# Kernel optimization log

Measured on AMD Instinct MI355X. Metric: run time of the kernel, lower is better.

The kernel has to match this reference:

```python
import jax, jax.numpy as jnp
import numpy as np

B, S, D, H = 2, 2048, 1024, 16
HD = D // H  # head_size = 64

def setup_inputs() -> dict:
    key = jax.random.key(0)
    ks = jax.random.split(key, 8)
    sc = 0.02
    return {
        "q": jax.random.normal(ks[0], (B, S, D), jnp.float32),
        "k": jax.random.normal(ks[1], (B, S, D), jnp.float32),
        "v": jax.random.normal(ks[2], (B, S, D), jnp.float32),
        "padding_mask": jnp.zeros((B, 1, 1, S), jnp.float32),
        "Wq": jax.random.normal(ks[3], (D, D), jnp.float32) * sc,
        "bq": jnp.zeros((D,), jnp.float32),
        "Wk": jax.random.normal(ks[4], (D, D), jnp.float32) * sc,
        "bk": jnp.zeros((D,), jnp.float32),
        "Wv": jax.random.normal(ks[5], (D, D), jnp.float32) * sc,
        "bv": jnp.zeros((D,), jnp.float32),
        "Wo": jax.random.normal(ks[6], (D, D), jnp.float32) * sc,
        "bo": jnp.zeros((D,), jnp.float32),
    }

def reference(q, k, v, padding_mask, Wq, bq, Wk, bk, Wv, bv, Wo, bo):
    b = q.shape[0]
    qh = (q @ Wq + bq).reshape(b, -1, H, HD)
    kh = (k @ Wk + bk).reshape(b, -1, H, HD)
    vh = (v @ Wv + bv).reshape(b, -1, H, HD)
    # [B, H, Sq, Sk] scores, materialized as in the original
    qk = jnp.einsum('bjhd,bkhd->bhjk', qh, kh) / jnp.sqrt(jnp.float32(HD))
    qk = qk + padding_mask * -1e12
    attn = jax.nn.softmax(qk, axis=-1)
    qkv = jnp.einsum('bhjk,bkhd->bjhd', attn, vh).reshape(b, -1, D)
    return qkv @ Wo + bo
```

## Files before the change

kernel.cpp:

```cpp
#include <hip/hip_runtime.h>
#include <math.h>

typedef __bf16 bf16_t;
typedef __bf16 bf16x8 __attribute__((ext_vector_type(8)));
typedef __bf16 bf16x4v __attribute__((ext_vector_type(4)));
typedef float f32x4 __attribute__((ext_vector_type(4)));
typedef float f32x16 __attribute__((ext_vector_type(16)));

#define LOG2E 1.4426950408889634f
#define MBIAS_C (-1e12f * LOG2E)

#if __has_builtin(__builtin_amdgcn_exp2f)
#define EXP2F(x) __builtin_amdgcn_exp2f(x)
#else
#define EXP2F(x) exp2f(x)
#endif

typedef __attribute__((address_space(1))) const unsigned int g_u32;
typedef __attribute__((address_space(3))) unsigned int l_u32;
__device__ __forceinline__ void load_lds_16B(const void* g, void* l){
  __builtin_amdgcn_global_load_lds((g_u32*)g, (l_u32*)l, 16, 0, 0);
}

__device__ __forceinline__ f32x16 zero16(){
  f32x16 z;
  #pragma unroll
  for (int i = 0; i < 16; i++) z[i] = 0.f;
  return z;
}

typedef union { bf16x4v b4; uint2 u2; } pk8;
typedef union { uint2 h[2]; bf16x8 b8; } pk16;
typedef union { float4 f4[4]; f32x16 v; } cinit_t;

__global__ __launch_bounds__(256) void cast3_kernel(const float* __restrict__ q,
                                                    const float* __restrict__ k,
                                                    const float* __restrict__ v,
                                                    bf16_t* __restrict__ out){
  int z = blockIdx.y;
  const float* x = (z == 0) ? q : (z == 1) ? k : v;
  int i = blockIdx.x * 256 + threadIdx.x;
  float4 f = reinterpret_cast<const float4*>(x)[i];
  bf16x4v w;
  w[0] = (bf16_t)f.x; w[1] = (bf16_t)f.y; w[2] = (bf16_t)f.z; w[3] = (bf16_t)f.w;
  reinterpret_cast<bf16x4v*>(out + (size_t)z * 4194304)[i] = w;
}

__global__ __launch_bounds__(256) void mask_scale_kernel(const float* __restrict__ mask,
                                                         float* __restrict__ ms){
  int i = blockIdx.x * 256 + threadIdx.x;
  ms[i] = mask[i] * MBIAS_C;
}

__global__ __launch_bounds__(256) void wtrans4_kernel(const float* __restrict__ Wq,
                                                      const float* __restrict__ Wk,
                                                      const float* __restrict__ Wv,
                                                      const float* __restrict__ Wo,
                                                      bf16_t* __restrict__ Wcat,
                                                      bf16_t* __restrict__ Wot){
  __shared__ float T[32][33];
  int z = blockIdx.z;
  const float* W = (z == 0) ? Wq : (z == 1) ? Wk : (z == 2) ? Wv : Wo;
  bf16_t* dst = (z < 3) ? (Wcat + (size_t)z * 1024 * 1024) : Wot;
  int x = threadIdx.x, y = threadIdx.y;
  int k0 = blockIdx.y * 32, n0 = blockIdx.x * 32;
  #pragma unroll
  for (int i = 0; i < 4; i++) T[y + 8*i][x] = W[(size_t)(k0 + y + 8*i) * 1024 + n0 + x];
  __syncthreads();
  #pragma unroll
  for (int i = 0; i < 4; i++) dst[(size_t)(n0 + y + 8*i) * 1024 + k0 + x] = (bf16_t)T[x][y + 8*i];
}

__device__ __forceinline__ void qkv_epilogue(f32x4 (&acc)[4][4], int seg, int n0g, int m0,
                                             int wm, int wn, int l16, int lq,
                                             const float* bias, bf16_t* qp, bf16_t* kp,
                                             bf16_t* vh){
  bf16_t* Cp = (seg == 0) ? qp : (seg == 1) ? kp : vh;
  float scale = (seg == 0) ? 0.125f * LOG2E : 1.0f;
  #pragma unroll
  for (int ti = 0; ti < 4; ti++){
    #pragma unroll
    for (int tj = 0; tj < 4; tj++){
      int col = (n0g + wn + tj*16 + l16) & 1023;
      float bvv = bias[col];
      #pragma unroll
      for (int r = 0; r < 4; r++){
        int row = m0 + wm + ti*16 + lq*4 + r;
        Cp[(size_t)row * 1024 + col] = (bf16_t)((acc[ti][tj][r] + bvv) * scale);
      }
    }
  }
}

__global__ __launch_bounds__(256) void gemm_qkv_bf(const bf16_t* __restrict__ qkvin,
                                                   const bf16_t* __restrict__ Wcat,
                                                   const float* __restrict__ bq,
                                                   const float* __restrict__ bk,
                                                   const float* __restrict__ bv,
                                                   bf16_t* __restrict__ qp,
                                                   bf16_t* __restrict__ kp,
                                                   bf16_t* __restrict__ vh){
  const int K = 1024;
  __shared__ __align__(16) bf16_t As[128*32];
  __shared__ __align__(16) bf16_t Bs[128*32];
  int tid = threadIdx.x, wave = tid >> 6, lane = tid & 63;
  int l16 = lane & 15, lq = lane >> 4;
  int n0g = blockIdx.x * 128;
  int seg = n0g >> 10;
  const bf16_t* A   = qkvin + (size_t)seg * 4194304;
  const float* bias = (seg == 0) ? bq : (seg == 1) ? bk : bv;
  int m0 = blockIdx.y * 128;
  int wm = (wave >> 1) * 64, wn = (wave & 1) * 64;
  int cposR = lq ^ ((l16 >> 2) & 3);
  f32x4 acc[4][4] = {};
  for (int kt = 0; kt < K; kt += 32){
    __syncthreads();
    #pragma unroll
    for (int i = 0; i < 2; i++){
      int u = tid + 256*i;
      int r = u >> 2, cpos = u & 3, cg = cpos ^ ((r >> 2) & 3);
      int ldsoff = (wave*64 + 256*i) * 16;
      load_lds_16B(&A[(size_t)(m0 + r) * K + kt + cg*8], (char*)As + ldsoff);
      load_lds_16B(&Wcat[(size_t)(n0g + r) * K + kt + cg*8], (char*)Bs + ldsoff);
    }
    __syncthreads();
    bf16x8 af[4], bfr[4];
    #pragma unroll
    for (int t = 0; t < 4; t++) af[t]  = *reinterpret_cast<bf16x8*>(&As[(wm + t*16 + l16)*32 + cposR*8]);
    #pragma unroll
    for (int t = 0; t < 4; t++) bfr[t] = *reinterpret_cast<bf16x8*>(&Bs[(wn + t*16 + l16)*32 + cposR*8]);
    #pragma unroll
    for (int ti = 0; ti < 4; ti++)
      #pragma unroll
      for (int tj = 0; tj < 4; tj++)
        acc[ti][tj] = __builtin_amdgcn_mfma_f32_16x16x32_bf16(af[ti], bfr[tj], acc[ti][tj], 0, 0, 0);
  }
  qkv_epilogue(acc, seg, n0g, m0, wm, wn, l16, lq, bias, qp, kp, vh);
}

__global__ __launch_bounds__(256) void gemm_qkv_f32(const float* __restrict__ qi,
                                                    const float* __restrict__ ki,
                                                    const float* __restrict__ vi,
                                                    const bf16_t* __restrict__ Wcat,
                                                    const float* __restrict__ bq,
                                                    const float* __restrict__ bk,
                                                    const float* __restrict__ bv,
                                                    bf16_t* __restrict__ qp,
                                                    bf16_t* __restrict__ kp,
                                                    bf16_t* __restrict__ vh){
  const int K = 1024;
  __shared__ __align__(16) float  Asf[128*32];
  __shared__ __align__(16) bf16_t Bs[128*32];
  int tid = threadIdx.x, wave = tid >> 6, lane = tid & 63;
  int l16 = lane & 15, lq = lane >> 4;
  int n0g = blockIdx.x * 128;
  int seg = n0g >> 10;
  const float* A    = (seg == 0) ? qi : (seg == 1) ? ki : vi;
  const float* bias = (seg == 0) ? bq : (seg == 1) ? bk : bv;
  int m0 = blockIdx.y * 128;
  int wm = (wave >> 1) * 64, wn = (wave & 1) * 64;
  int cposR = lq ^ ((l16 >> 2) & 3);
  int ca0 = (2*lq)     ^ (l16 & 7);
  int ca1 = (2*lq + 1) ^ (l16 & 7);
  f32x4 acc[4][4] = {};
  for (int kt = 0; kt < K; kt += 32){
    __syncthreads();
    #pragma unroll
    for (int i = 0; i < 4; i++){
      int u = tid + 256*i;
      int r = u >> 3, cpos = u & 7, cg = cpos ^ (r & 7);
      load_lds_16B(&A[(size_t)(m0 + r) * K + kt + cg*4], (char*)Asf + (wave*64 + 256*i)*16);
    }
    #pragma unroll
    for (int i = 0; i < 2; i++){
      int u = tid + 256*i;
      int r = u >> 2, cpos = u & 3, cg = cpos ^ ((r >> 2) & 3);
      load_lds_16B(&Wcat[(size_t)(n0g + r) * K + kt + cg*8], (char*)Bs + (wave*64 + 256*i)*16);
    }
    __syncthreads();
    bf16x8 af[4], bfr[4];
    #pragma unroll
    for (int t = 0; t < 4; t++){
      int row = wm + t*16 + l16;
      f32x4 x0 = *reinterpret_cast<f32x4*>(&Asf[row*32 + ca0*4]);
      f32x4 x1 = *reinterpret_cast<f32x4*>(&Asf[row*32 + ca1*4]);
      bf16x8 a;
      a[0] = (bf16_t)x0[0]; a[1] = (bf16_t)x0[1]; a[2] = (bf16_t)x0[2]; a[3] = (bf16_t)x0[3];
      a[4] = (bf16_t)x1[0]; a[5] = (bf16_t)x1[1]; a[6] = (bf16_t)x1[2]; a[7] = (bf16_t)x1[3];
      af[t] = a;
    }
    #pragma unroll
    for (int t = 0; t < 4; t++) bfr[t] = *reinterpret_cast<bf16x8*>(&Bs[(wn + t*16 + l16)*32 + cposR*8]);
    #pragma unroll
    for (int ti = 0; ti < 4; ti++)
      #pragma unroll
      for (int tj = 0; tj < 4; tj++)
        acc[ti][tj] = __builtin_amdgcn_mfma_f32_16x16x32_bf16(af[ti], bfr[tj], acc[ti][tj], 0, 0, 0);
  }
  qkv_epilogue(acc, seg, n0g, m0, wm, wn, l16, lq, bias, qp, kp, vh);
}

__global__ __launch_bounds__(256) void gemm_out(const bf16_t* __restrict__ A,
                                                const bf16_t* __restrict__ Bt,
                                                const float* __restrict__ bias,
                                                float* __restrict__ C){
  const int K = 1024, N = 1024;
  __shared__ __align__(16) bf16_t As[128*64];
  __shared__ __align__(16) bf16_t Bs[64*64];
  int tid = threadIdx.x, wave = tid >> 6, lane = tid & 63;
  int l16 = lane & 15, lq = lane >> 4;
  int m0 = blockIdx.y * 128, n0 = blockIdx.x * 64;
  int wm = wave * 32;
  f32x4 acc[2][4] = {};
  for (int kt = 0; kt < K; kt += 64){
    __syncthreads();
    #pragma unroll
    for (int i = 0; i < 4; i++){
      int u = tid + 256*i;
      int r = u >> 3, cpos = u & 7, cg = cpos ^ (r & 7);
      load_lds_16B(&A[(size_t)(m0 + r) * K + kt + cg*8], (char*)As + (wave*64 + 256*i)*16);
    }
    #pragma unroll
    for (int i = 0; i < 2; i++){
      int u = tid + 256*i;
      int r = u >> 3, cpos = u & 7, cg = cpos ^ (r & 7);
      load_lds_16B(&Bt[(size_t)(n0 + r) * K + kt + cg*8], (char*)Bs + (wave*64 + 256*i)*16);
    }
    __syncthreads();
    #pragma unroll
    for (int kk = 0; kk < 2; kk++){
      bf16x8 af[2], bfr[4];
      #pragma unroll
      for (int t = 0; t < 2; t++){
        int row = wm + t*16 + l16, cpos = (kk*4 + lq) ^ (l16 & 7);
        af[t] = *reinterpret_cast<bf16x8*>(&As[row*64 + cpos*8]);
      }
      #pragma unroll
      for (int t = 0; t < 4; t++){
        int row = t*16 + l16, cpos = (kk*4 + lq) ^ (l16 & 7);
        bfr[t] = *reinterpret_cast<bf16x8*>(&Bs[row*64 + cpos*8]);
      }
      #pragma unroll
      for (int ti = 0; ti < 2; ti++)
        #pragma unroll
        for (int tj = 0; tj < 4; tj++)
          acc[ti][tj] = __builtin_amdgcn_mfma_f32_16x16x32_bf16(af[ti], bfr[tj], acc[ti][tj], 0, 0, 0);
    }
  }
  #pragma unroll
  for (int ti = 0; ti < 2; ti++){
    #pragma unroll
    for (int tj = 0; tj < 4; tj++){
      int col = n0 + tj*16 + l16;
      float bvv = bias[col];
      #pragma unroll
      for (int r = 0; r < 4; r++){
        int row = m0 + wm + ti*16 + lq*4 + r;
        C[(size_t)row * N + col] = acc[ti][tj][r] + bvv;
      }
    }
  }
}

__global__ __launch_bounds__(256) void vtrans_kernel(const bf16_t* __restrict__ vh,
                                                     bf16_t* __restrict__ Vt){
  __shared__ bf16_t T[64][72];
  int tid = threadIdx.x;
  int s0 = blockIdx.x * 64, h = blockIdx.y, b = blockIdx.z;
  #pragma unroll
  for (int i = 0; i < 2; i++){
    int u = tid + 256*i;
    int r = u >> 3, c = (u & 7) * 8;
    *reinterpret_cast<uint4*>(&T[r][c]) =
      *reinterpret_cast<const uint4*>(&vh[(size_t)(b*2048 + s0 + r) * 1024 + h*64 + c]);
  }
  __syncthreads();
  #pragma unroll
  for (int i = 0; i < 2; i++){
    int u = tid + 256*i;
    int d = u >> 3, cs = (u & 7) * 8;
    bf16_t t8[8];
    #pragma unroll
    for (int j = 0; j < 8; j++) t8[j] = T[cs + j][d];
    *reinterpret_cast<uint4*>(&Vt[(size_t)((b*16 + h)*64 + d) * 2048 + s0 + cs]) =
      *reinterpret_cast<uint4*>(t8);
  }
}

__global__ __launch_bounds__(256, 4) void attn_kernel(const bf16_t* __restrict__ qp,
                                                      const bf16_t* __restrict__ kp,
                                                      const bf16_t* __restrict__ vt,
                                                      const float* __restrict__ ms,
                                                      bf16_t* __restrict__ ctx){
  const int S = 2048, D = 1024, HD = 64;
  __shared__ __align__(16) char smem[33024];
  float* Lsum  = (float*)(smem + 32768);
  float* Opart = (float*)smem;
  int tid = threadIdx.x, wave = tid >> 6, lane = tid & 63;
  int l32 = lane & 31, H = lane >> 5;
  int qhalf = wave & 1, khalf = wave >> 1;
  int qt = blockIdx.x, h = blockIdx.y, b = blockIdx.z;
  const bf16_t* Qg = qp + (size_t)b*S*D + h*HD;
  const bf16_t* Kg = kp + (size_t)b*S*D + h*HD;
  const bf16_t* Vg = vt + (size_t)(b*16 + h)*HD*S;
  const float*  Mg = ms + (size_t)b*S;

  auto stage = [&](int kt, int bsel){
    char* Kd = smem + bsel*8192;
    char* Vd = smem + 16384 + bsel*8192;
    #pragma unroll
    for (int i = 0; i < 2; i++){
      int u = tid + 256*i;
      int r = u >> 3, c = u & 7, cg = c ^ (r & 7);
      int ldsoff = (wave*64 + 256*i) * 16;
      load_lds_16B(&Kg[(size_t)(kt + r) * D + cg*8], Kd + ldsoff);
      load_lds_16B(&Vg[(size_t)r * S + kt + cg*8], Vd + ldsoff);
    }
  };

  int qrow = qt*64 + qhalf*32 + l32;
  bf16x8 qf[4];
  #pragma unroll
  for (int s = 0; s < 4; s++)
    qf[s] = *reinterpret_cast<const bf16x8*>(&Qg[(size_t)qrow * D + s*16 + 8*H]);

  f32x16 o0 = zero16(), o1 = zero16(), lmm = zero16();
  int krow = khalf*32 + l32;

  pk16 ones;
  ones.h[0].x = 0x3F803F80u; ones.h[0].y = 0x3F803F80u;
  ones.h[1].x = 0x3F803F80u; ones.h[1].y = 0x3F803F80u;

  stage(0, 0);
  __syncthreads();
  int cur = 0;

  for (int kt = 0; kt < S; kt += 64){
    cinit_t ci;
    #pragma unroll
    for (int g = 0; g < 4; g++)
      ci.f4[g] = *reinterpret_cast<const float4*>(&Mg[kt + khalf*32 + 8*g + 4*H]);

    if (kt + 64 < S) stage(kt + 64, cur ^ 1);

    bf16_t* Ks  = (bf16_t*)(smem + cur*8192);
    bf16_t* Vts = (bf16_t*)(smem + 16384 + cur*8192);

    f32x16 sc;
    #pragma unroll
    for (int s = 0; s < 4; s++){
      int cp = (2*s + H) ^ (l32 & 7);
      bf16x8 kf = *reinterpret_cast<bf16x8*>(&Ks[krow*64 + cp*8]);
      if (s == 0) sc = __builtin_amdgcn_mfma_f32_32x32x16_bf16(kf, qf[0], ci.v, 0, 0, 0);
      else        sc = __builtin_amdgcn_mfma_f32_32x32x16_bf16(kf, qf[s], sc, 0, 0, 0);
    }
    pk8 grp[4];
    #pragma unroll
    for (int g = 0; g < 4; g++){
      float p0 = EXP2F(sc[4*g+0]);
      float p1 = EXP2F(sc[4*g+1]);
      float p2 = EXP2F(sc[4*g+2]);
      float p3 = EXP2F(sc[4*g+3]);
      pk8 w;
      w.b4[0] = (bf16_t)p0; w.b4[1] = (bf16_t)p1; w.b4[2] = (bf16_t)p2; w.b4[3] = (bf16_t)p3;
      grp[g] = w;
    }
    #pragma unroll
    for (int kk = 0; kk < 2; kk++){
      uint2 ga = grp[2*kk].u2;
      uint2 gb = grp[2*kk+1].u2;
      uint2 send = H ? ga : gb;
      uint2 recv;
      recv.x = (unsigned)__shfl_xor((int)send.x, 32);
      recv.y = (unsigned)__shfl_xor((int)send.y, 32);
      pk16 fr;
      fr.h[0] = H ? recv : ga;
      fr.h[1] = H ? gb : recv;
      int cp = (4*khalf + 2*kk + H) ^ (l32 & 7);
      bf16x8 vf0 = *reinterpret_cast<bf16x8*>(&Vts[l32*64 + cp*8]);
      bf16x8 vf1 = *reinterpret_cast<bf16x8*>(&Vts[(32 + l32)*64 + cp*8]);
      o0  = __builtin_amdgcn_mfma_f32_32x32x16_bf16(fr.b8, vf0, o0, 0, 0, 0);
      o1  = __builtin_amdgcn_mfma_f32_32x32x16_bf16(fr.b8, vf1, o1, 0, 0, 0);
      lmm = __builtin_amdgcn_mfma_f32_32x32x16_bf16(fr.b8, ones.b8, lmm, 0, 0, 0);
    }
    __syncthreads();
    cur ^= 1;
  }

  if (khalf == 1){
    #pragma unroll
    for (int reg = 0; reg < 16; reg++){
      Opart[qhalf*2048 + reg*64 + lane]        = o0[reg];
      Opart[qhalf*2048 + 1024 + reg*64 + lane] = o1[reg];
    }
    if (l32 == 0){
      #pragma unroll
      for (int reg = 0; reg < 16; reg++)
        Lsum[qhalf*32 + (reg & 3) + 8*(reg >> 2) + 4*H] = lmm[reg];
    }
  }
  __syncthreads();
  if (khalf == 0){
    #pragma unroll
    for (int reg = 0; reg < 16; reg++){
      o0[reg] += Opart[qhalf*2048 + reg*64 + lane];
      o1[reg] += Opart[qhalf*2048 + 1024 + reg*64 + lane];
    }
    #pragma unroll
    for (int g = 0; g < 4; g++){
      #pragma unroll
      for (int r = 0; r < 4; r++){
        float lf = lmm[4*g + r] + Lsum[qhalf*32 + 8*g + 4*H + r];
        float inv = 1.f / lf;
        int grow = qt*64 + qhalf*32 + 8*g + 4*H + r;
        size_t base = (size_t)(b*S + grow) * D + h*HD;
        ctx[base + l32]      = (bf16_t)(o0[4*g + r] * inv);
        ctx[base + 32 + l32] = (bf16_t)(o1[4*g + r] * inv);
      }
    }
  }
}

extern "C" void kernel_launch(void* const* d_in, const int* in_sizes, int n_in,
                              void* d_out, int out_size, void* d_ws, size_t ws_size,
                              hipStream_t stream){
  const float* q    = (const float*)d_in[0];
  const float* k    = (const float*)d_in[1];
  const float* v    = (const float*)d_in[2];
  const float* mask = (const float*)d_in[3];
  const float* Wq   = (const float*)d_in[4];
  const float* bq   = (const float*)d_in[5];
  const float* Wk   = (const float*)d_in[6];
  const float* bk   = (const float*)d_in[7];
  const float* Wv   = (const float*)d_in[8];
  const float* bv   = (const float*)d_in[9];
  const float* Wo   = (const float*)d_in[10];
  const float* bo   = (const float*)d_in[11];

  char* ws = (char*)d_ws;
  bf16_t* qp    = (bf16_t*)(ws);
  bf16_t* kp    = (bf16_t*)(ws + 8388608);
  bf16_t* vh    = (bf16_t*)(ws + 16777216);
  bf16_t* Wcat  = (bf16_t*)(ws + 25165824);
  bf16_t* Wot   = (bf16_t*)(ws + 31457280);
  bf16_t* Vt    = (bf16_t*)(ws + 33554432);
  bf16_t* ctx   = (bf16_t*)(ws + 41943040);
  bf16_t* qkvin = (bf16_t*)(ws + 33554432);
  float*  msbuf = (float*)(ws + 16777216);

  wtrans4_kernel<<<dim3(32,32,4), dim3(32,8), 0, stream>>>(Wq, Wk, Wv, Wo, Wcat, Wot);
  if (ws_size >= 58720256){
    cast3_kernel<<<dim3(4096,3), 256, 0, stream>>>(q, k, v, qkvin);
    gemm_qkv_bf<<<dim3(24,32), 256, 0, stream>>>(qkvin, Wcat, bq, bk, bv, qp, kp, vh);
  } else {
    gemm_qkv_f32<<<dim3(24,32), 256, 0, stream>>>(q, k, v, Wcat, bq, bk, bv, qp, kp, vh);
  }
  vtrans_kernel<<<dim3(32,16,2), 256, 0, stream>>>(vh, Vt);
  mask_scale_kernel<<<dim3(16), 256, 0, stream>>>(mask, msbuf);
  attn_kernel<<<dim3(32,16,2), 256, 0, stream>>>(qp, kp, Vt, msbuf, ctx);
  gemm_out<<<dim3(16,32), 256, 0, stream>>>(ctx, Wot, bo, (float*)d_out);
}
```

Measured before the change: 239.3 us.

## Process two 64-row query tiles per attention block to reuse K/V fragments

Each attention block now handles 128 query rows as two 64-row subtiles. The K and V fragments read from LDS are shared across both subtiles, which halves the K/V global staging traffic per query row. The grid is halved to match. Launch bounds drop to 2 blocks per CU because the doubled accumulators and Q fragments raise register use, so there are fewer waves available to hide latency.

```diff
diff --git a/kernel.cpp b/kernel.cpp
--- a/kernel.cpp
+++ b/kernel.cpp
@@ -287,13 +287,13 @@
   }
 }
 
-__global__ __launch_bounds__(256, 4) void attn_kernel(const bf16_t* __restrict__ qp,
+__global__ __launch_bounds__(256, 2) void attn_kernel(const bf16_t* __restrict__ qp,
                                                       const bf16_t* __restrict__ kp,
                                                       const bf16_t* __restrict__ vt,
                                                       const float* __restrict__ ms,
                                                       bf16_t* __restrict__ ctx){
   const int S = 2048, D = 1024, HD = 64;
-  __shared__ __align__(16) char smem[33024];
+  __shared__ __align__(16) char smem[33280];
   float* Lsum  = (float*)(smem + 32768);
   float* Opart = (float*)smem;
   int tid = threadIdx.x, wave = tid >> 6, lane = tid & 63;
@@ -318,13 +318,18 @@
     }
   };
 
-  int qrow = qt*64 + qhalf*32 + l32;
-  bf16x8 qf[4];
-  #pragma unroll
-  for (int s = 0; s < 4; s++)
-    qf[s] = *reinterpret_cast<const bf16x8*>(&Qg[(size_t)qrow * D + s*16 + 8*H]);
-
-  f32x16 o0 = zero16(), o1 = zero16(), lmm = zero16();
+  bf16x8 qf[2][4];
+  #pragma unroll
+  for (int j = 0; j < 2; j++){
+    int qrow = qt*128 + j*64 + qhalf*32 + l32;
+    #pragma unroll
+    for (int s = 0; s < 4; s++)
+      qf[j][s] = *reinterpret_cast<const bf16x8*>(&Qg[(size_t)qrow * D + s*16 + 8*H]);
+  }
+
+  f32x16 o0[2], o1[2], lmm[2];
+  #pragma unroll
+  for (int j = 0; j < 2; j++){ o0[j] = zero16(); o1[j] = zero16(); lmm[j] = zero16(); }
   int krow = khalf*32 + l32;
 
   pk16 ones;
@@ -346,42 +351,52 @@
     bf16_t* Ks  = (bf16_t*)(smem + cur*8192);
     bf16_t* Vts = (bf16_t*)(smem + 16384 + cur*8192);
 
-    f32x16 sc;
+    bf16x8 kf[4];
     #pragma unroll
     for (int s = 0; s < 4; s++){
       int cp = (2*s + H) ^ (l32 & 7);
-      bf16x8 kf = *reinterpret_cast<bf16x8*>(&Ks[krow*64 + cp*8]);
-      if (s == 0) sc = __builtin_amdgcn_mfma_f32_32x32x16_bf16(kf, qf[0], ci.v, 0, 0, 0);
-      else        sc = __builtin_amdgcn_mfma_f32_32x32x16_bf16(kf, qf[s], sc, 0, 0, 0);
-    }
-    pk8 grp[4];
-    #pragma unroll
-    for (int g = 0; g < 4; g++){
-      float p0 = EXP2F(sc[4*g+0]);
-      float p1 = EXP2F(sc[4*g+1]);
-      float p2 = EXP2F(sc[4*g+2]);
-      float p3 = EXP2F(sc[4*g+3]);
-      pk8 w;
-      w.b4[0] = (bf16_t)p0; w.b4[1] = (bf16_t)p1; w.b4[2] = (bf16_t)p2; w.b4[3] = (bf16_t)p3;
-      grp[g] = w;
-    }
+      kf[s] = *reinterpret_cast<bf16x8*>(&Ks[krow*64 + cp*8]);
+    }
+
+    pk8 grp[2][4];
+    #pragma unroll
+    for (int j = 0; j < 2; j++){
+      f32x16 sc = __builtin_amdgcn_mfma_f32_32x32x16_bf16(kf[0], qf[j][0], ci.v, 0, 0, 0);
+      #pragma unroll
+      for (int s = 1; s < 4; s++)
+        sc = __builtin_amdgcn_mfma_f32_32x32x16_bf16(kf[s], qf[j][s], sc, 0, 0, 0);
+      #pragma unroll
+      for (int g = 0; g < 4; g++){
+        float p0 = EXP2F(sc[4*g+0]);
+        float p1 = EXP2F(sc[4*g+1]);
+        float p2 = EXP2F(sc[4*g+2]);
+        float p3 = EXP2F(sc[4*g+3]);
+        pk8 w;
+        w.b4[0] = (bf16_t)p0; w.b4[1] = (bf16_t)p1; w.b4[2] = (bf16_t)p2; w.b4[3] = (bf16_t)p3;
+        grp[j][g] = w;
+      }
+    }
+
     #pragma unroll
     for (int kk = 0; kk < 2; kk++){
-      uint2 ga = grp[2*kk].u2;
-      uint2 gb = grp[2*kk+1].u2;
-      uint2 send = H ? ga : gb;
-      uint2 recv;
-      recv.x = (unsigned)__shfl_xor((int)send.x, 32);
-      recv.y = (unsigned)__shfl_xor((int)send.y, 32);
-      pk16 fr;
-      fr.h[0] = H ? recv : ga;
-      fr.h[1] = H ? gb : recv;
       int cp = (4*khalf + 2*kk + H) ^ (l32 & 7);
       bf16x8 vf0 = *reinterpret_cast<bf16x8*>(&Vts[l32*64 + cp*8]);
       bf16x8 vf1 = *reinterpret_cast<bf16x8*>(&Vts[(32 + l32)*64 + cp*8]);
-      o0  = __builtin_amdgcn_mfma_f32_32x32x16_bf16(fr.b8, vf0, o0, 0, 0, 0);
-      o1  = __builtin_amdgcn_mfma_f32_32x32x16_bf16(fr.b8, vf1, o1, 0, 0, 0);
-      lmm = __builtin_amdgcn_mfma_f32_32x32x16_bf16(fr.b8, ones.b8, lmm, 0, 0, 0);
+      #pragma unroll
+      for (int j = 0; j < 2; j++){
+        uint2 ga = grp[j][2*kk].u2;
+        uint2 gb = grp[j][2*kk+1].u2;
+        uint2 send = H ? ga : gb;
+        uint2 recv;
+        recv.x = (unsigned)__shfl_xor((int)send.x, 32);
+        recv.y = (unsigned)__shfl_xor((int)send.y, 32);
+        pk16 fr;
+        fr.h[0] = H ? recv : ga;
+        fr.h[1] = H ? gb : recv;
+        o0[j]  = __builtin_amdgcn_mfma_f32_32x32x16_bf16(fr.b8, vf0, o0[j], 0, 0, 0);
+        o1[j]  = __builtin_amdgcn_mfma_f32_32x32x16_bf16(fr.b8, vf1, o1[j], 0, 0, 0);
+        lmm[j] = __builtin_amdgcn_mfma_f32_32x32x16_bf16(fr.b8, ones.b8, lmm[j], 0, 0, 0);
+      }
     }
     __syncthreads();
     cur ^= 1;
@@ -389,33 +404,39 @@
 
   if (khalf == 1){
     #pragma unroll
-    for (int reg = 0; reg < 16; reg++){
-      Opart[qhalf*2048 + reg*64 + lane]        = o0[reg];
-      Opart[qhalf*2048 + 1024 + reg*64 + lane] = o1[reg];
-    }
-    if (l32 == 0){
-      #pragma unroll
-      for (int reg = 0; reg < 16; reg++)
-        Lsum[qhalf*32 + (reg & 3) + 8*(reg >> 2) + 4*H] = lmm[reg];
+    for (int j = 0; j < 2; j++){
+      #pragma unroll
+      for (int reg = 0; reg < 16; reg++){
+        Opart[(j*2 + qhalf)*2048 + reg*64 + lane]        = o0[j][reg];
+        Opart[(j*2 + qhalf)*2048 + 1024 + reg*64 + lane] = o1[j][reg];
+      }
+      if (l32 == 0){
+        #pragma unroll
+        for (int reg = 0; reg < 16; reg++)
+          Lsum[j*64 + qhalf*32 + (reg & 3) + 8*(reg >> 2) + 4*H] = lmm[j][reg];
+      }
     }
   }
   __syncthreads();
   if (khalf == 0){
     #pragma unroll
-    for (int reg = 0; reg < 16; reg++){
-      o0[reg] += Opart[qhalf*2048 + reg*64 + lane];
-      o1[reg] += Opart[qhalf*2048 + 1024 + reg*64 + lane];
-    }
-    #pragma unroll
-    for (int g = 0; g < 4; g++){
-      #pragma unroll
-      for (int r = 0; r < 4; r++){
-        float lf = lmm[4*g + r] + Lsum[qhalf*32 + 8*g + 4*H + r];
-        float inv = 1.f / lf;
-        int grow = qt*64 + qhalf*32 + 8*g + 4*H + r;
-        size_t base = (size_t)(b*S + grow) * D + h*HD;
-        ctx[base + l32]      = (bf16_t)(o0[4*g + r] * inv);
-        ctx[base + 32 + l32] = (bf16_t)(o1[4*g + r] * inv);
+    for (int j = 0; j < 2; j++){
+      #pragma unroll
+      for (int reg = 0; reg < 16; reg++){
+        o0[j][reg] += Opart[(j*2 + qhalf)*2048 + reg*64 + lane];
+        o1[j][reg] += Opart[(j*2 + qhalf)*2048 + 1024 + reg*64 + lane];
+      }
+      #pragma unroll
+      for (int g = 0; g < 4; g++){
+        #pragma unroll
+        for (int r = 0; r < 4; r++){
+          float lf = lmm[j][4*g + r] + Lsum[j*64 + qhalf*32 + 8*g + 4*H + r];
+          float inv = 1.f / lf;
+          int grow = qt*128 + j*64 + qhalf*32 + 8*g + 4*H + r;
+          size_t base = (size_t)(b*S + grow) * D + h*HD;
+          ctx[base + l32]      = (bf16_t)(o0[j][4*g + r] * inv);
+          ctx[base + 32 + l32] = (bf16_t)(o1[j][4*g + r] * inv);
+        }
       }
     }
   }
@@ -457,6 +478,6 @@
   }
   vtrans_kernel<<<dim3(32,16,2), 256, 0, stream>>>(vh, Vt);
   mask_scale_kernel<<<dim3(16), 256, 0, stream>>>(mask, msbuf);
-  attn_kernel<<<dim3(32,16,2), 256, 0, stream>>>(qp, kp, Vt, msbuf, ctx);
+  attn_kernel<<<dim3(16,16,2), 256, 0, stream>>>(qp, kp, Vt, msbuf, ctx);
   gemm_out<<<dim3(16,32), 256, 0, stream>>>(ctx, Wot, bo, (float*)d_out);
 }
```

Result: no change. 235.3 us (-1.6%).
